# Optimization experiments

Measured on AMD Instinct MI355X. Metric: run time of the kernel, lower is better.

Reference implementation:

```python
import jax, jax.numpy as jnp
import numpy as np

D_MODEL, HID, N_NODES, NODE_DIM = 128, 256, 17, 32

def _gelu(x):
    return jax.nn.gelu(x, approximate=False)  # torch nn.GELU default (erf)

def setup_inputs() -> dict:
    key = jax.random.key(0)
    ks = jax.random.split(key, 12)
    B, W = 16, 4096
    x = jax.random.normal(ks[0], (B, W, D_MODEL), dtype=jnp.float32)
    # node_proj: Linear(128,256) -> GELU -> Linear(256, 17*32)
    W1 = jax.random.normal(ks[1], (D_MODEL, HID), dtype=jnp.float32) / np.sqrt(D_MODEL)
    b1 = jnp.zeros((HID,), jnp.float32)
    W2 = jax.random.normal(ks[2], (HID, N_NODES * NODE_DIM), dtype=jnp.float32) / np.sqrt(HID)
    b2 = jnp.zeros((N_NODES * NODE_DIM,), jnp.float32)
    # GAT1
    adj1 = jnp.eye(N_NODES, dtype=jnp.float32) * 5.0 + jax.random.normal(ks[3], (N_NODES, N_NODES), jnp.float32) * 0.05
    Wg1 = jax.random.normal(ks[4], (NODE_DIM, NODE_DIM), dtype=jnp.float32) / np.sqrt(NODE_DIM)
    bg1 = jnp.zeros((NODE_DIM,), jnp.float32)
    # GAT2
    adj2 = jnp.eye(N_NODES, dtype=jnp.float32) * 5.0 + jax.random.normal(ks[5], (N_NODES, N_NODES), jnp.float32) * 0.05
    Wg2 = jax.random.normal(ks[6], (NODE_DIM, NODE_DIM), dtype=jnp.float32) / np.sqrt(NODE_DIM)
    bg2 = jnp.zeros((NODE_DIM,), jnp.float32)
    # coord_proj: Linear(32, 2)
    Wc = jax.random.normal(ks[7], (NODE_DIM, 2), dtype=jnp.float32) / np.sqrt(NODE_DIM)
    bc = jnp.zeros((2,), jnp.float32)
    return {"x": x, "W1": W1, "b1": b1, "W2": W2, "b2": b2,
            "adj1": adj1, "Wg1": Wg1, "bg1": bg1,
            "adj2": adj2, "Wg2": Wg2, "bg2": bg2,
            "Wc": Wc, "bc": bc}

def _gat(nodes, adj_logits, Wg, bg):
    # nodes: [B, W, N, F]
    adj = jax.nn.softmax(adj_logits, axis=-1)          # [N, N]
    mixed = jnp.einsum('ij,bwjf->bwif', adj, nodes)    # graph conv over 17 joints
    return _gelu(mixed @ Wg + bg) + nodes              # linear-GELU + residual

def reference(x, W1, b1, W2, b2, adj1, Wg1, bg1, adj2, Wg2, bg2, Wc, bc):
    B, W, _ = x.shape
    h = _gelu(x @ W1 + b1)                 # [B, W, 256] (dropout inactive at eval)
    nodes = (h @ W2 + b2).reshape(B, W, N_NODES, NODE_DIM)
    out = _gat(nodes, adj1, Wg1, bg1)
    out = _gat(out, adj2, Wg2, bg2)
    return out @ Wc + bc                   # [B, W, 17, 2]
```

## Files before the change

### kernel.cpp

```cpp
#include <hip/hip_runtime.h>
#include <hip/hip_bf16.h>

using bf16 = __hip_bfloat16;
typedef __bf16 bf16x4v __attribute__((ext_vector_type(4)));
typedef __bf16 bf16x8 __attribute__((ext_vector_type(8)));
typedef float f32x4 __attribute__((ext_vector_type(4)));

#define MT 32
#define SX 136
#define SH 264
#define SJ 20
#define TFS 640
#define NTF_ELEMS 20480
#define MS_BASE 20496
#define SMS 36
#define MSW 1224
#define S_ELEMS 30800

__device__ __forceinline__ float bf2f(bf16 v) { return __bfloat162float(v); }

__device__ __forceinline__ float gelu_f(float x) {
    float z  = x * fmaf(0.10294343f * x, x, 2.3022082f);
    float t  = fmaf(-2.0f, __builtin_amdgcn_rcpf(exp2f(z) + 1.0f), 1.0f);
    float hx = 0.5f * x;
    return fmaf(hx, t, hx);
}

__device__ __forceinline__ bf16x8 ld8(const bf16* p) {
    return *reinterpret_cast<const bf16x8*>(p);
}
__device__ __forceinline__ bf16x8 ld8u(const bf16* p) {
    bf16x4v lo = *reinterpret_cast<const bf16x4v*>(p);
    bf16x4v hi = *reinterpret_cast<const bf16x4v*>(p + 4);
    return __builtin_shufflevector(lo, hi, 0, 1, 2, 3, 4, 5, 6, 7);
}
__device__ __forceinline__ f32x4 mfma16(bf16x8 a, bf16x8 b, f32x4 c) {
    return __builtin_amdgcn_mfma_f32_16x16x32_bf16(a, b, c, 0, 0, 0);
}

__global__ void prep_kernel(const float* __restrict__ W1, const float* __restrict__ W2,
                            const float* __restrict__ Wg1, const float* __restrict__ Wg2,
                            const float* __restrict__ adj1, const float* __restrict__ adj2,
                            bf16* __restrict__ w1t, bf16* __restrict__ w2t,
                            bf16* __restrict__ wg1t, bf16* __restrict__ wg2t,
                            float* __restrict__ A1f, float* __restrict__ A2f) {
    int idx = blockIdx.x * 256 + threadIdx.x;
    if (idx < 32768) {
        int r = idx >> 8, c = idx & 255;
        w1t[c * 128 + r] = __float2bfloat16(W1[idx]);
    } else if (idx < 172032) {
        int j = idx - 32768;
        int r = j / 544, c = j % 544;
        w2t[c * 256 + r] = __float2bfloat16(W2[j]);
    } else if (idx < 173056) {
        int j = idx - 172032;
        wg1t[(j & 31) * 32 + (j >> 5)] = __float2bfloat16(Wg1[j]);
    } else if (idx < 174080) {
        int j = idx - 173056;
        wg2t[(j & 31) * 32 + (j >> 5)] = __float2bfloat16(Wg2[j]);
    }
    if (blockIdx.x == 0) {
        int t = threadIdx.x;
        if (t < 17 || (t >= 32 && t < 49)) {
            const float* adj = (t < 17) ? adj1 : adj2;
            float*       A   = (t < 17) ? A1f  : A2f;
            int row = (t < 17) ? t : (t - 32);
            float v[17]; float mx = -1e30f;
            for (int j = 0; j < 17; ++j) { v[j] = adj[row * 17 + j]; mx = fmaxf(mx, v[j]); }
            float s = 0.0f;
            for (int j = 0; j < 17; ++j) { v[j] = __expf(v[j] - mx); s += v[j]; }
            float inv = 1.0f / s;
            for (int j = 0; j < 17; ++j) A[row * 17 + j] = v[j] * inv;
        }
    }
}

__global__ void prep_mixb(const float* __restrict__ A1f, const float* __restrict__ A2f,
                          bf16* __restrict__ mb) {
    int idx = blockIdx.x * 256 + threadIdx.x;
    if (idx < 2048) {
        int g = idx >> 10, rem = idx & 1023;
        int nt = rem >> 9, lane = (rem >> 3) & 63, e = rem & 7;
        int i = nt * 16 + (lane & 15);
        int j = (lane >> 4) * 8 + e;
        const float* A = g ? A2f : A1f;
        float v = (i < 17 && j < 17) ? A[i * 17 + j] : 0.0f;
        mb[idx] = __float2bfloat16(v);
    }
}

__global__ __launch_bounds__(512, 4)
void gat_main(const float* __restrict__ x,
              const float* __restrict__ b1, const float* __restrict__ b2,
              const float* __restrict__ bg1, const float* __restrict__ bg2,
              const bf16* __restrict__ w1t, const bf16* __restrict__ w2t,
              const bf16* __restrict__ wg1t, const bf16* __restrict__ wg2t,
              const bf16* __restrict__ mb,
              const float* __restrict__ Wc, const float* __restrict__ bc,
              float* __restrict__ out) {
    __shared__ alignas(16) bf16 S[S_ELEMS];
    bf16* xs = S;
    bf16* hs = S + 4352;

    const int tid  = threadIdx.x;
    const int w    = tid >> 6;
    const int lane = tid & 63;
    const int l    = lane & 15;
    const int q    = lane >> 4;
    const int t0   = blockIdx.x * MT;

    for (int c = tid; c < 1024; c += 512) {
        int row = c >> 5, c4 = c & 31;
        const float4 v = *reinterpret_cast<const float4*>(x + (size_t)(t0 + row) * 128 + c4 * 4);
        bf16 tmp[4] = { __float2bfloat16(v.x), __float2bfloat16(v.y),
                        __float2bfloat16(v.z), __float2bfloat16(v.w) };
        *reinterpret_cast<ushort4*>(xs + row * SX + c4 * 4) =
            *reinterpret_cast<const ushort4*>(tmp);
    }
    __syncthreads();

    for (int nt = w * 2; nt < w * 2 + 2; ++nt) {
        int n = nt * 16 + l;
        bf16x8 bfr[4];
        const bf16* wp = w1t + n * 128 + q * 8;
#pragma unroll
        for (int kf = 0; kf < 4; ++kf) bfr[kf] = ld8(wp + kf * 32);
        float bias = b1[n];
#pragma unroll
        for (int mt = 0; mt < 2; ++mt) {
            f32x4 acc = {0.f, 0.f, 0.f, 0.f};
            const bf16* ap = xs + (mt * 16 + l) * SX + q * 8;
#pragma unroll
            for (int kf = 0; kf < 4; ++kf)
                acc = mfma16(ld8(ap + kf * 32), bfr[kf], acc);
            int trow = mt * 16 + q * 4;
#pragma unroll
            for (int r = 0; r < 4; ++r)
                hs[(trow + r) * SH + n] = __float2bfloat16(gelu_f(acc[r] + bias));
        }
    }
    __syncthreads();

    {
        bf16x8 af[2][8];
#pragma unroll
        for (int mt = 0; mt < 2; ++mt)
#pragma unroll
            for (int kf = 0; kf < 8; ++kf)
                af[mt][kf] = ld8(hs + (mt * 16 + l) * SH + kf * 32 + q * 8);
        __syncthreads();

        for (int z = tid; z < 3072; z += 512) {
            int row = z / 3, k = z - row * 3;
            S[row * SJ + 17 + k] = __float2bfloat16(0.f);
        }
        if (tid < 16) S[NTF_ELEMS + tid] = __float2bfloat16(0.f);

        for (int nt = w; nt < 34; nt += 8) {
            int n = nt * 16 + l;
            float bias = b2[n];
            int i = n >> 5, f = n & 31;
            f32x4 a0 = {0.f, 0.f, 0.f, 0.f}, a1 = {0.f, 0.f, 0.f, 0.f};
            const bf16* wp = w2t + n * 256 + q * 8;
#pragma unroll
            for (int kf = 0; kf < 8; ++kf) {
                bf16x8 bfr = ld8(wp + kf * 32);
                a0 = mfma16(af[0][kf], bfr, a0);
                a1 = mfma16(af[1][kf], bfr, a1);
            }
#pragma unroll
            for (int mt = 0; mt < 2; ++mt) {
                const f32x4 acc = mt ? a1 : a0;
#pragma unroll
                for (int r = 0; r < 4; ++r) {
                    int t = mt * 16 + q * 4 + r;
                    S[t * TFS + f * SJ + i] = __float2bfloat16(acc[r] + bias);
                }
            }
        }
    }
    __syncthreads();

    bf16* ms_p = S + MS_BASE + w * MSW;

    for (int g = 0; g < 2; ++g) {
        const bf16* mbg = mb + g * 1024;
        const bf16* wgt = g ? wg2t : wg1t;
        const float* bg = g ? bg2 : bg1;

        bf16x8 mixB[2] = { ld8(mbg + lane * 8), ld8(mbg + 512 + lane * 8) };
        bf16x8 wfr[2];
#pragma unroll
        for (int nt = 0; nt < 2; ++nt) wfr[nt] = ld8(wgt + (nt * 16 + l) * 32 + q * 8);
        float bgf[2] = { bg[l], bg[16 + l] };

        for (int p = 0; p < 2; ++p) {
            const int T0 = w * 4 + p * 2;

#pragma unroll
            for (int u = 0; u < 4; ++u) {
                int tl = u >> 1, ft = u & 1;
                int R = (T0 + tl) * 32 + ft * 16 + l;
                bf16x8 afr = ld8u(S + R * SJ + q * 8);
                int f0 = ft * 16 + q * 4;
#pragma unroll
                for (int nt = 0; nt < 2; ++nt) {
                    f32x4 acc = {0.f, 0.f, 0.f, 0.f};
                    acc = mfma16(afr, mixB[nt], acc);
                    union { ushort4 u4; bf16 b[4]; } pk;
#pragma unroll
                    for (int r = 0; r < 4; ++r) pk.b[r] = __float2bfloat16(acc[r]);
                    if (nt == 0) {
                        *reinterpret_cast<ushort4*>(ms_p + (tl * 16 + l) * SMS + f0) = pk.u4;
                    } else if (l == 0) {
                        *reinterpret_cast<ushort4*>(ms_p + (32 + tl) * SMS + f0) = pk.u4;
                    }
                }
            }

#pragma unroll
            for (int mt = 0; mt < 3; ++mt) {
                bf16x8 afr = ld8u(ms_p + (mt * 16 + l) * SMS + q * 8);
#pragma unroll
                for (int nt = 0; nt < 2; ++nt) {
                    f32x4 acc = {0.f, 0.f, 0.f, 0.f};
                    acc = mfma16(afr, wfr[nt], acc);
                    int fp = nt * 16 + l;
                    if (mt < 2) {
                        int i0 = q * 4;
                        bf16* ptr = S + (T0 + mt) * TFS + fp * SJ + i0;
                        union { ushort4 u4; bf16 b[4]; } old, nw;
                        old.u4 = *reinterpret_cast<const ushort4*>(ptr);
#pragma unroll
                        for (int r = 0; r < 4; ++r) {
                            float v = gelu_f(acc[r] + bgf[nt]) + bf2f(old.b[r]);
                            nw.b[r] = __float2bfloat16(v);
                        }
                        *reinterpret_cast<ushort4*>(ptr) = nw.u4;
                    } else if (q == 0) {
#pragma unroll
                        for (int r = 0; r < 2; ++r) {
                            bf16* pp = S + (T0 + r) * TFS + fp * SJ + 16;
                            float v = gelu_f(acc[r] + bgf[nt]) + bf2f(*pp);
                            *pp = __float2bfloat16(v);
                        }
                    }
                }
            }
        }
    }

    for (int s = lane; s < 68; s += 64) {
        int tl = s / 17, i = s - tl * 17;
        int t  = w * 4 + tl;
        const bf16* gp = S + t * TFS + i;
        float o0 = bc[0], o1 = bc[1];
#pragma unroll
        for (int f = 0; f < 32; ++f) {
            float v = bf2f(gp[f * SJ]);
            o0 = fmaf(v, Wc[f * 2 + 0], o0);
            o1 = fmaf(v, Wc[f * 2 + 1], o1);
        }
        float2 pr = { o0, o1 };
        reinterpret_cast<float2*>(out)[(size_t)(t0 + t) * 17 + i] = pr;
    }
}

extern "C" void kernel_launch(void* const* d_in, const int* in_sizes, int n_in,
                              void* d_out, int out_size, void* d_ws, size_t ws_size,
                              hipStream_t stream) {
    const float* x    = (const float*)d_in[0];
    const float* W1   = (const float*)d_in[1];
    const float* b1   = (const float*)d_in[2];
    const float* W2   = (const float*)d_in[3];
    const float* b2   = (const float*)d_in[4];
    const float* adj1 = (const float*)d_in[5];
    const float* Wg1  = (const float*)d_in[6];
    const float* bg1  = (const float*)d_in[7];
    const float* adj2 = (const float*)d_in[8];
    const float* Wg2  = (const float*)d_in[9];
    const float* bg2  = (const float*)d_in[10];
    const float* Wc   = (const float*)d_in[11];
    const float* bc   = (const float*)d_in[12];

    char* ws = (char*)d_ws;
    bf16*  w1t  = (bf16*)(ws + 0);
    bf16*  w2t  = (bf16*)(ws + 65536);
    bf16*  wg1t = (bf16*)(ws + 344064);
    bf16*  wg2t = (bf16*)(ws + 346112);
    float* A1f  = (float*)(ws + 348160);
    float* A2f  = (float*)(ws + 349376);
    bf16*  mbt  = (bf16*)(ws + 350592);

    prep_kernel<<<680, 256, 0, stream>>>(W1, W2, Wg1, Wg2, adj1, adj2,
                                         w1t, w2t, wg1t, wg2t, A1f, A2f);
    prep_mixb<<<8, 256, 0, stream>>>(A1f, A2f, mbt);

    const int tokens = 16 * 4096;
    gat_main<<<tokens / MT, 512, 0, stream>>>(x, b1, b2, bg1, bg2,
                                              w1t, w2t, wg1t, wg2t, mbt,
                                              Wc, bc, (float*)d_out);
}
```

Measured before the change: 218.1 us.

## Fold first GAT layer's adjacency mix and linear into precomposed W2 weights

The first graph layer is linear before its GELU, so the adjacency softmax, Wg1 and bg1 are pre-folded into a second 256x544 weight matrix and bias. The main kernel computes nodes and the GAT1 pre-activation in the same MFMA loop and applies GELU plus residual on the spot, leaving only the second GAT layer as a per-node pass. The two prep kernels are merged into one, which also builds the composed weights. This doubles the W2-stage MFMA work and weight traffic in exchange for removing one full mix/linear stage, and rounding the composed weights to bf16 adds some precision error.

```diff
diff --git a/kernel.cpp b/kernel.cpp
--- a/kernel.cpp
+++ b/kernel.cpp
@@ -38,32 +38,19 @@
     return __builtin_amdgcn_mfma_f32_16x16x32_bf16(a, b, c, 0, 0, 0);
 }
 
-__global__ void prep_kernel(const float* __restrict__ W1, const float* __restrict__ W2,
-                            const float* __restrict__ Wg1, const float* __restrict__ Wg2,
-                            const float* __restrict__ adj1, const float* __restrict__ adj2,
-                            bf16* __restrict__ w1t, bf16* __restrict__ w2t,
-                            bf16* __restrict__ wg1t, bf16* __restrict__ wg2t,
-                            float* __restrict__ A1f, float* __restrict__ A2f) {
-    int idx = blockIdx.x * 256 + threadIdx.x;
-    if (idx < 32768) {
-        int r = idx >> 8, c = idx & 255;
-        w1t[c * 128 + r] = __float2bfloat16(W1[idx]);
-    } else if (idx < 172032) {
-        int j = idx - 32768;
-        int r = j / 544, c = j % 544;
-        w2t[c * 256 + r] = __float2bfloat16(W2[j]);
-    } else if (idx < 173056) {
-        int j = idx - 172032;
-        wg1t[(j & 31) * 32 + (j >> 5)] = __float2bfloat16(Wg1[j]);
-    } else if (idx < 174080) {
-        int j = idx - 173056;
-        wg2t[(j & 31) * 32 + (j >> 5)] = __float2bfloat16(Wg2[j]);
-    }
-    if (blockIdx.x == 0) {
+__global__ void megaprep(const float* __restrict__ W1, const float* __restrict__ W2,
+                         const float* __restrict__ Wg1, const float* __restrict__ Wg2,
+                         const float* __restrict__ adj1, const float* __restrict__ adj2,
+                         const float* __restrict__ b2, const float* __restrict__ bg1,
+                         bf16* __restrict__ w1t, bf16* __restrict__ w2t,
+                         bf16* __restrict__ w2g, bf16* __restrict__ wg2t,
+                         bf16* __restrict__ mb2, float* __restrict__ bb1) {
+    __shared__ float A1s[289], A2s[289];
+    {
         int t = threadIdx.x;
         if (t < 17 || (t >= 32 && t < 49)) {
             const float* adj = (t < 17) ? adj1 : adj2;
-            float*       A   = (t < 17) ? A1f  : A2f;
+            float*       A   = (t < 17) ? A1s  : A2s;
             int row = (t < 17) ? t : (t - 32);
             float v[17]; float mx = -1e30f;
             for (int j = 0; j < 17; ++j) { v[j] = adj[row * 17 + j]; mx = fmaxf(mx, v[j]); }
@@ -73,29 +60,63 @@
             for (int j = 0; j < 17; ++j) A[row * 17 + j] = v[j] * inv;
         }
     }
-}
-
-__global__ void prep_mixb(const float* __restrict__ A1f, const float* __restrict__ A2f,
-                          bf16* __restrict__ mb) {
+    __syncthreads();
+
     int idx = blockIdx.x * 256 + threadIdx.x;
-    if (idx < 2048) {
-        int g = idx >> 10, rem = idx & 1023;
-        int nt = rem >> 9, lane = (rem >> 3) & 63, e = rem & 7;
+    if (idx < 32768) {
+        int n = idx >> 7, k = idx & 127;
+        w1t[idx] = __float2bfloat16(W1[k * 256 + n]);
+    } else if (idx < 172032) {
+        int o = idx - 32768;
+        int n = o >> 8, k = o & 255;
+        w2t[o] = __float2bfloat16(W2[k * 544 + n]);
+    } else if (idx < 311296) {
+        int o = idx - 172032;
+        int np = o >> 8, k = o & 255;
+        int i = np >> 5, fp = np & 31;
+        const float* wrow = W2 + k * 544;
+        float acc = 0.0f;
+        for (int j = 0; j < 17; ++j) {
+            float aj = A1s[i * 17 + j];
+            float t = 0.0f;
+            for (int f = 0; f < 32; ++f)
+                t = fmaf(Wg1[f * 32 + fp], wrow[j * 32 + f], t);
+            acc = fmaf(aj, t, acc);
+        }
+        w2g[o] = __float2bfloat16(acc);
+    } else if (idx < 312320) {
+        int o = idx - 311296;
+        int fp = o >> 5, f = o & 31;
+        wg2t[o] = __float2bfloat16(Wg2[f * 32 + fp]);
+    } else if (idx < 313344) {
+        int o = idx - 312320;
+        int nt = o >> 9, lane = (o >> 3) & 63, e = o & 7;
         int i = nt * 16 + (lane & 15);
         int j = (lane >> 4) * 8 + e;
-        const float* A = g ? A2f : A1f;
-        float v = (i < 17 && j < 17) ? A[i * 17 + j] : 0.0f;
-        mb[idx] = __float2bfloat16(v);
+        float v = (i < 17 && j < 17) ? A2s[i * 17 + j] : 0.0f;
+        mb2[o] = __float2bfloat16(v);
+    } else if (idx < 313888) {
+        int np = idx - 313344;
+        int i = np >> 5, fp = np & 31;
+        float acc = bg1[fp];
+        for (int j = 0; j < 17; ++j) {
+            float aj = A1s[i * 17 + j];
+            float t = 0.0f;
+            for (int f = 0; f < 32; ++f)
+                t = fmaf(Wg1[f * 32 + fp], b2[j * 32 + f], t);
+            acc = fmaf(aj, t, acc);
+        }
+        bb1[np] = acc;
     }
 }
 
 __global__ __launch_bounds__(512, 4)
 void gat_main(const float* __restrict__ x,
               const float* __restrict__ b1, const float* __restrict__ b2,
-              const float* __restrict__ bg1, const float* __restrict__ bg2,
+              const float* __restrict__ bg2, const float* __restrict__ bb1,
               const bf16* __restrict__ w1t, const bf16* __restrict__ w2t,
-              const bf16* __restrict__ wg1t, const bf16* __restrict__ wg2t,
-              const bf16* __restrict__ mb,
+              const bf16* __restrict__ w2g, const bf16* __restrict__ wg2t,
+              const bf16* __restrict__ mb2,
               const float* __restrict__ Wc, const float* __restrict__ bc,
               float* __restrict__ out) {
     __shared__ alignas(16) bf16 S[S_ELEMS];
@@ -150,31 +171,42 @@
                 af[mt][kf] = ld8(hs + (mt * 16 + l) * SH + kf * 32 + q * 8);
         __syncthreads();
 
-        for (int z = tid; z < 3072; z += 512) {
-            int row = z / 3, k = z - row * 3;
-            S[row * SJ + 17 + k] = __float2bfloat16(0.f);
+        for (int rowz = tid; rowz < 1024; rowz += 512) {
+            int base = rowz * SJ + 17;
+            S[base]     = __float2bfloat16(0.f);
+            S[base + 1] = __float2bfloat16(0.f);
+            S[base + 2] = __float2bfloat16(0.f);
         }
         if (tid < 16) S[NTF_ELEMS + tid] = __float2bfloat16(0.f);
 
         for (int nt = w; nt < 34; nt += 8) {
             int n = nt * 16 + l;
-            float bias = b2[n];
+            float bias2 = b2[n];
+            float biasP = bb1[n];
             int i = n >> 5, f = n & 31;
             f32x4 a0 = {0.f, 0.f, 0.f, 0.f}, a1 = {0.f, 0.f, 0.f, 0.f};
+            f32x4 c0 = {0.f, 0.f, 0.f, 0.f}, c1 = {0.f, 0.f, 0.f, 0.f};
             const bf16* wp = w2t + n * 256 + q * 8;
+            const bf16* gp = w2g + n * 256 + q * 8;
 #pragma unroll
             for (int kf = 0; kf < 8; ++kf) {
                 bf16x8 bfr = ld8(wp + kf * 32);
                 a0 = mfma16(af[0][kf], bfr, a0);
                 a1 = mfma16(af[1][kf], bfr, a1);
+                bf16x8 gfr = ld8(gp + kf * 32);
+                c0 = mfma16(af[0][kf], gfr, c0);
+                c1 = mfma16(af[1][kf], gfr, c1);
             }
 #pragma unroll
             for (int mt = 0; mt < 2; ++mt) {
-                const f32x4 acc = mt ? a1 : a0;
+                const f32x4 accN = mt ? a1 : a0;
+                const f32x4 accP = mt ? c1 : c0;
 #pragma unroll
                 for (int r = 0; r < 4; ++r) {
                     int t = mt * 16 + q * 4 + r;
-                    S[t * TFS + f * SJ + i] = __float2bfloat16(acc[r] + bias);
+                    float nodesv = accN[r] + bias2;
+                    float v = gelu_f(accP[r] + biasP) + nodesv;
+                    S[t * TFS + f * SJ + i] = __float2bfloat16(v);
                 }
             }
         }
@@ -183,16 +215,12 @@
 
     bf16* ms_p = S + MS_BASE + w * MSW;
 
-    for (int g = 0; g < 2; ++g) {
-        const bf16* mbg = mb + g * 1024;
-        const bf16* wgt = g ? wg2t : wg1t;
-        const float* bg = g ? bg2 : bg1;
-
-        bf16x8 mixB[2] = { ld8(mbg + lane * 8), ld8(mbg + 512 + lane * 8) };
+    {
+        bf16x8 mixB[2] = { ld8(mb2 + lane * 8), ld8(mb2 + 512 + lane * 8) };
         bf16x8 wfr[2];
 #pragma unroll
-        for (int nt = 0; nt < 2; ++nt) wfr[nt] = ld8(wgt + (nt * 16 + l) * 32 + q * 8);
-        float bgf[2] = { bg[l], bg[16 + l] };
+        for (int nt = 0; nt < 2; ++nt) wfr[nt] = ld8(wg2t + (nt * 16 + l) * 32 + q * 8);
+        float bgf[2] = { bg2[l], bg2[16 + l] };
 
         for (int p = 0; p < 2; ++p) {
             const int T0 = w * 4 + p * 2;
@@ -286,18 +314,16 @@
     char* ws = (char*)d_ws;
     bf16*  w1t  = (bf16*)(ws + 0);
     bf16*  w2t  = (bf16*)(ws + 65536);
-    bf16*  wg1t = (bf16*)(ws + 344064);
-    bf16*  wg2t = (bf16*)(ws + 346112);
-    float* A1f  = (float*)(ws + 348160);
-    float* A2f  = (float*)(ws + 349376);
-    bf16*  mbt  = (bf16*)(ws + 350592);
-
-    prep_kernel<<<680, 256, 0, stream>>>(W1, W2, Wg1, Wg2, adj1, adj2,
-                                         w1t, w2t, wg1t, wg2t, A1f, A2f);
-    prep_mixb<<<8, 256, 0, stream>>>(A1f, A2f, mbt);
+    bf16*  w2g  = (bf16*)(ws + 344064);
+    bf16*  wg2t = (bf16*)(ws + 622592);
+    bf16*  mb2  = (bf16*)(ws + 624640);
+    float* bb1  = (float*)(ws + 626688);
+
+    megaprep<<<1227, 256, 0, stream>>>(W1, W2, Wg1, Wg2, adj1, adj2, b2, bg1,
+                                       w1t, w2t, w2g, wg2t, mb2, bb1);
 
     const int tokens = 16 * 4096;
-    gat_main<<<tokens / MT, 512, 0, stream>>>(x, b1, b2, bg1, bg2,
-                                              w1t, w2t, wg1t, wg2t, mbt,
+    gat_main<<<tokens / MT, 512, 0, stream>>>(x, b1, b2, bg2, bb1,
+                                              w1t, w2t, w2g, wg2t, mb2,
                                               Wc, bc, (float*)d_out);
 }
```

After: 311.1 us. 42.6% more time.
